# Kernel optimization log

Measured on AMD Instinct MI355X. Metric: run time of the kernel, lower is better.

## Reference

```python
import jax, jax.numpy as jnp
import numpy as np
from jax import lax

WIN = 7            # win_size -> (7,7,7) window in 3d mode
NPIX = WIN ** 3    # 343
K1, K2 = 0.01, 0.03
COV_NORM = NPIX / (NPIX - 1)
DN = ('NCDHW', 'OIDHW', 'NCDHW')


def _box3d(x):
    """Separable uniform (box) mean filter, VALID padding. Same math as
    conv3d with a ones(wt,ws,ws)/NPIX kernel, but O(win) per voxel per axis."""
    kd = jnp.ones((1, 1, WIN, 1, 1), x.dtype)
    kh = jnp.ones((1, 1, 1, WIN, 1), x.dtype)
    kw = jnp.ones((1, 1, 1, 1, WIN), x.dtype)
    x = lax.conv_general_dilated(x, kd, (1, 1, 1), 'VALID', dimension_numbers=DN)
    x = lax.conv_general_dilated(x, kh, (1, 1, 1), 'VALID', dimension_numbers=DN)
    x = lax.conv_general_dilated(x, kw, (1, 1, 1), 'VALID', dimension_numbers=DN)
    return x / NPIX


def setup_inputs() -> dict:
    key = jax.random.key(0)
    k1, k2, k3 = jax.random.split(key, 3)
    shape = (4, 1, 32, 320, 320)  # [B, C=1, T, H, W]
    pred = jax.random.normal(k1, shape, dtype=jnp.float32)
    targ = jax.random.normal(k2, shape, dtype=jnp.float32)
    data_range = jax.random.uniform(k3, (4,), dtype=jnp.float32)
    return {'pred': pred, 'targ': targ, 'data_range': data_range}


def reference(pred, targ, data_range):
    dr = data_range[:, None, None, None, None].astype(pred.dtype)
    C1 = (K1 * dr) ** 2
    C2 = (K2 * dr) ** 2
    ux = _box3d(pred)
    uy = _box3d(targ)
    uxx = _box3d(pred * pred)
    uyy = _box3d(targ * targ)
    uxy = _box3d(pred * targ)
    vx = COV_NORM * (uxx - ux * ux)
    vy = COV_NORM * (uyy - uy * uy)
    vxy = COV_NORM * (uxy - ux * uy)
    A1 = 2 * ux * uy + C1
    A2 = 2 * vxy + C2
    B1 = ux ** 2 + uy ** 2 + C1
    B2 = vx + vy + C2
    S = (A1 * A2) / (B1 * B2)
    return (1 - S).mean()
```

## Files before the change

kernel.cpp:

```cpp
#include <hip/hip_runtime.h>


#define NPIX 343

constexpr int B = 4, T = 32, H = 320, W = 320;
constexpr int TO = T - 6, HO = H - 6, WO = W - 6;
constexpr long long NOUT = (long long)B * TO * HO * WO;

constexpr int TH = 16, TW = 26;
constexpr int IH = 22, IWP = 16;
constexpr int NTH = 20, NTW = 13;
constexpr int NS = 32;

typedef float v2f __attribute__((ext_vector_type(2)));

template<int N>
__device__ __forceinline__ float row_shr(float x) {
    return __int_as_float(__builtin_amdgcn_update_dpp(
        0, __float_as_int(x), 0x110 | N, 0xF, 0xF, true));
}

__global__ __launch_bounds__(256) void ssim3d_fused(
    const float* __restrict__ pred,
    const float* __restrict__ targ,
    const float* __restrict__ drange,
    double* __restrict__ acc)
{
    __shared__ float4 spq[2][IH][IWP];
    __shared__ float wsum[4];

    const int bx = blockIdx.x;
    const int b  = bx / (NTH * NTW);
    int rem      = bx % (NTH * NTW);
    const int h0 = (rem / NTW) * TH;
    const int w0 = (rem % NTW) * TW;

    const int tid = threadIdx.x;
    const int oh  = tid >> 4;
    const int k   = tid & 15;

    const float* pb = pred + (long long)b * T * H * W;
    const float* qb = targ + (long long)b * T * H * W;

    const int r0 = tid >> 4, c0 = tid & 15;
    const int gr0 = min(h0 + r0, H - 1), gc0 = min(w0 + 2 * c0, W - 2);
    const float* g0p = pb + (long long)gr0 * W + gc0;
    const float* g0q = qb + (long long)gr0 * W + gc0;

    const bool act1 = (tid < 96);
    const int r1 = 16 + (tid >> 4), c1 = tid & 15;
    const int gr1 = min(h0 + r1, H - 1), gc1 = min(w0 + 2 * c1, W - 2);
    const float* g1p = pb + (long long)gr1 * W + gc1;
    const float* g1q = qb + (long long)gr1 * W + gc1;

    float2 d0p, d0q, d1p, d1q;
    auto prefetchw = [&](int s) {
        const long long so = (long long)s * H * W;
        d0p = *reinterpret_cast<const float2*>(g0p + so);
        d0q = *reinterpret_cast<const float2*>(g0q + so);
        if (act1) {
            d1p = *reinterpret_cast<const float2*>(g1p + so);
            d1q = *reinterpret_cast<const float2*>(g1q + so);
        }
    };
    auto commitw = [&](int buf) {
        spq[buf][r0][c0] = make_float4(d0p.x, d0p.y, d0q.x, d0q.y);
        if (act1) spq[buf][r1][c1] = make_float4(d1p.x, d1p.y, d1q.x, d1q.y);
    };

    const bool vh = (h0 + oh < HO);
    const bool k3 = (k >= 3);
    const bool vE = k3 && vh && (w0 + 2 * k - 6 < WO);
    const bool vO = k3 && vh && (w0 + 2 * k - 5 < WO);

    const float dr  = drange[b];
    const float C1s = (0.01f * dr) * (0.01f * dr);
    const float C2s = (0.03f * dr) * (0.03f * dr);
    const float inv  = 1.0f / (float)NPIX;
    const float covn = (float)NPIX / (float)(NPIX - 1);
    const v2f invv  = {inv, inv};
    const v2f C1vv  = {C1s, C1s};
    const v2f C2vv  = {C2s, C2s};
    const v2f covnv = {covn, covn};
    const v2f c2cov = {2.f * covn, 2.f * covn};

    v2f rEO[4][7], tEO[4];
#pragma unroll
    for (int f = 0; f < 4; ++f) {
        tEO[f] = (v2f){0.f, 0.f};
#pragma unroll
        for (int j = 0; j < 7; ++j) rEO[f][j] = (v2f){0.f, 0.f};
    }
    float loss = 0.f;

    auto slice = [&](int s, int jj, bool doEmit, bool doCommit, bool doPrefetch) {
        const int bs = s & 1, bn = bs ^ 1;

        if (doCommit)  commitw(bn);
        if (doPrefetch) prefetchw(s + 2);

        v2f c0 = {0.f, 0.f}, c1v = {0.f, 0.f}, c2 = {0.f, 0.f}, c3 = {0.f, 0.f};
#pragma unroll
        for (int dy = 0; dy < 7; ++dy) {
            float4 v = spq[bs][oh + dy][k];
            v2f vp = {v.x, v.y};
            v2f vq = {v.z, v.w};
            c0 += vp;
            c1v += vq;
            c2 = __builtin_elementwise_fma(vp, vp, c2);
            c2 = __builtin_elementwise_fma(vq, vq, c2);
            c3 = __builtin_elementwise_fma(vp, vq, c3);
        }

        __syncthreads();

        v2f sv[4];
        {
            v2f cf[4] = {c0, c1v, c2, c3};
#pragma unroll
            for (int f = 0; f < 4; ++f) {
                float ps = cf[f].x + cf[f].y;
                float t1 = ps + row_shr<1>(ps);
                float s8 = t1 + row_shr<2>(t1);
                float eL = row_shr<3>(cf[f].x);
                sv[f].x = s8 - cf[f].y;
                sv[f].y = s8 - eL;
            }
        }

#pragma unroll
        for (int f = 0; f < 4; ++f) {
            tEO[f] += sv[f] - rEO[f][jj];
            rEO[f][jj] = sv[f];
        }

        if (doEmit) {
            v2f ux  = tEO[0] * invv;
            v2f uy  = tEO[1] * invv;
            v2f u2  = tEO[2] * invv;
            v2f uxy = tEO[3] * invv;
            v2f m   = __builtin_elementwise_fma(-ux, uy, uxy);
            v2f A2  = __builtin_elementwise_fma(c2cov, m, C2vv);
            v2f nb  = __builtin_elementwise_fma(-ux, ux, u2);
            nb      = __builtin_elementwise_fma(-uy, uy, nb);
            v2f B2  = __builtin_elementwise_fma(covnv, nb, C2vv);
            v2f ux2 = ux + ux;
            v2f A1  = __builtin_elementwise_fma(ux2, uy, C1vv);
            v2f B1  = __builtin_elementwise_fma(
                          ux, ux, __builtin_elementwise_fma(uy, uy, C1vv));
            v2f num = A1 * A2;
            v2f den = B1 * B2;
            float sx = __fdividef(num.x, den.x);
            float sy = __fdividef(num.y, den.y);
            if (vE) loss += 1.f - sx;
            if (vO) loss += 1.f - sy;
        }
    };

    prefetchw(0);
    commitw(0);
    prefetchw(1);
    __syncthreads();

#pragma unroll
    for (int jj = 0; jj < 7; ++jj)
        slice(jj, jj, jj == 6, true, true);

    for (int a = 7; a <= 21; a += 7)
#pragma unroll
        for (int jj = 0; jj < 7; ++jj)
            slice(a + jj, jj, true, true, true);

    slice(28, 0, true, true, true);
    slice(29, 1, true, true, true);
    slice(30, 2, true, true, false);
    slice(31, 3, true, false, false);

    for (int off = 32; off > 0; off >>= 1)
        loss += __shfl_down(loss, off, 64);
    const int lane = tid & 63;
    const int wid  = tid >> 6;
    if (lane == 0) wsum[wid] = loss;
    __syncthreads();
    if (tid == 0) {
        float s = wsum[0] + wsum[1] + wsum[2] + wsum[3];
        atomicAdd(acc, (double)s);
    }
}

__global__ void ssim3d_finalize(const double* __restrict__ acc,
                                float* __restrict__ out)
{
    out[0] = (float)(acc[0] / (double)NOUT);
}

extern "C" void kernel_launch(void* const* d_in, const int* in_sizes, int n_in,
                              void* d_out, int out_size, void* d_ws, size_t ws_size,
                              hipStream_t stream)
{
    const float* pred   = (const float*)d_in[0];
    const float* targ   = (const float*)d_in[1];
    const float* drange = (const float*)d_in[2];
    float* out  = (float*)d_out;
    double* acc = (double*)d_ws;

    hipMemsetAsync(acc, 0, sizeof(double), stream);

    const int nblocks = B * NTH * NTW;
    ssim3d_fused<<<nblocks, 256, 0, stream>>>(pred, targ, drange, acc);
    ssim3d_finalize<<<1, 1, 0, stream>>>(acc, out);
}
```

Measured before the change: 72.44 us.

## Use four-slot LDS ring to process two slices per barrier with float4 staging

Grows the shared-memory slice buffer from two slots to four and processes two depth slices per phase, so the kernel needs only half as many block-wide barriers. Global staging switches from float2 loads spread over 256 threads to float4 loads done by 176 threads, which cuts the number of load instructions. In exchange, LDS per block roughly doubles, more loaded data stays live in registers, and the fully unrolled phase loop makes the code larger. Either could lower occupancy.

```diff
diff --git a/kernel.cpp b/kernel.cpp
--- a/kernel.cpp
+++ b/kernel.cpp
@@ -10,7 +10,6 @@
 constexpr int TH = 16, TW = 26;
 constexpr int IH = 22, IWP = 16;
 constexpr int NTH = 20, NTW = 13;
-constexpr int NS = 32;
 
 typedef float v2f __attribute__((ext_vector_type(2)));
 
@@ -26,7 +25,7 @@
     const float* __restrict__ drange,
     double* __restrict__ acc)
 {
-    __shared__ float4 spq[2][IH][IWP];
+    __shared__ float4 spq[4][IH][IWP];
     __shared__ float wsum[4];
 
     const int bx = blockIdx.x;
@@ -42,30 +41,39 @@
     const float* pb = pred + (long long)b * T * H * W;
     const float* qb = targ + (long long)b * T * H * W;
 
-    const int r0 = tid >> 4, c0 = tid & 15;
-    const int gr0 = min(h0 + r0, H - 1), gc0 = min(w0 + 2 * c0, W - 2);
-    const float* g0p = pb + (long long)gr0 * W + gc0;
-    const float* g0q = qb + (long long)gr0 * W + gc0;
-
-    const bool act1 = (tid < 96);
-    const int r1 = 16 + (tid >> 4), c1 = tid & 15;
-    const int gr1 = min(h0 + r1, H - 1), gc1 = min(w0 + 2 * c1, W - 2);
-    const float* g1p = pb + (long long)gr1 * W + gc1;
-    const float* g1q = qb + (long long)gr1 * W + gc1;
-
-    float2 d0p, d0q, d1p, d1q;
-    auto prefetchw = [&](int s) {
-        const long long so = (long long)s * H * W;
-        d0p = *reinterpret_cast<const float2*>(g0p + so);
-        d0q = *reinterpret_cast<const float2*>(g0q + so);
-        if (act1) {
-            d1p = *reinterpret_cast<const float2*>(g1p + so);
-            d1q = *reinterpret_cast<const float2*>(g1q + so);
-        }
-    };
-    auto commitw = [&](int buf) {
-        spq[buf][r0][c0] = make_float4(d0p.x, d0p.y, d0q.x, d0q.y);
-        if (act1) spq[buf][r1][c1] = make_float4(d1p.x, d1p.y, d1q.x, d1q.y);
+    const bool stager = (tid < 176);
+    const int rs = tid >> 3;
+    const int qc = tid & 7;
+    const int grs = min(h0 + rs, H - 1), gcs = min(w0 + 4 * qc, W - 4);
+    const float* gps = pb + (long long)grs * W + gcs;
+    const float* gqs = qb + (long long)grs * W + gcs;
+
+    float4 pA, qA, pB, qB;
+    auto loadA = [&](int s) {
+        if (stager) {
+            const long long so = (long long)s * H * W;
+            pA = *reinterpret_cast<const float4*>(gps + so);
+            qA = *reinterpret_cast<const float4*>(gqs + so);
+        }
+    };
+    auto loadB = [&](int s) {
+        if (stager) {
+            const long long so = (long long)s * H * W;
+            pB = *reinterpret_cast<const float4*>(gps + so);
+            qB = *reinterpret_cast<const float4*>(gqs + so);
+        }
+    };
+    auto commitA = [&](int buf) {
+        if (stager) {
+            spq[buf][rs][2 * qc]     = make_float4(pA.x, pA.y, qA.x, qA.y);
+            spq[buf][rs][2 * qc + 1] = make_float4(pA.z, pA.w, qA.z, qA.w);
+        }
+    };
+    auto commitB = [&](int buf) {
+        if (stager) {
+            spq[buf][rs][2 * qc]     = make_float4(pB.x, pB.y, qB.x, qB.y);
+            spq[buf][rs][2 * qc + 1] = make_float4(pB.z, pB.w, qB.z, qB.w);
+        }
     };
 
     const bool vh = (h0 + oh < HO);
@@ -93,16 +101,11 @@
     }
     float loss = 0.f;
 
-    auto slice = [&](int s, int jj, bool doEmit, bool doCommit, bool doPrefetch) {
-        const int bs = s & 1, bn = bs ^ 1;
-
-        if (doCommit)  commitw(bn);
-        if (doPrefetch) prefetchw(s + 2);
-
+    auto compute = [&](int buf, int jj, bool doEmit) {
         v2f c0 = {0.f, 0.f}, c1v = {0.f, 0.f}, c2 = {0.f, 0.f}, c3 = {0.f, 0.f};
 #pragma unroll
         for (int dy = 0; dy < 7; ++dy) {
-            float4 v = spq[bs][oh + dy][k];
+            float4 v = spq[buf][oh + dy][k];
             v2f vp = {v.x, v.y};
             v2f vq = {v.z, v.w};
             c0 += vp;
@@ -111,8 +114,6 @@
             c2 = __builtin_elementwise_fma(vq, vq, c2);
             c3 = __builtin_elementwise_fma(vp, vq, c3);
         }
-
-        __syncthreads();
 
         v2f sv[4];
         {
@@ -157,24 +158,38 @@
         }
     };
 
-    prefetchw(0);
-    commitw(0);
-    prefetchw(1);
+    auto phase = [&](int p, int jj0, int jj1, bool doEmit,
+                     bool doCommit, bool doPrefetch) {
+        const int s0 = 2 * p;
+        if (doCommit) {
+            commitA((s0 + 2) & 3);
+            commitB((s0 + 3) & 3);
+        }
+        if (doPrefetch) {
+            loadA(s0 + 4);
+            loadB(s0 + 5);
+        }
+        compute(s0 & 3, jj0, doEmit);
+        compute((s0 + 1) & 3, jj1, doEmit);
+        __syncthreads();
+    };
+
+    loadA(0);
+    loadB(1);
+    commitA(0);
+    commitB(1);
+    loadA(2);
+    loadB(3);
     __syncthreads();
 
 #pragma unroll
-    for (int jj = 0; jj < 7; ++jj)
-        slice(jj, jj, jj == 6, true, true);
-
-    for (int a = 7; a <= 21; a += 7)
-#pragma unroll
-        for (int jj = 0; jj < 7; ++jj)
-            slice(a + jj, jj, true, true, true);
-
-    slice(28, 0, true, true, true);
-    slice(29, 1, true, true, true);
-    slice(30, 2, true, true, false);
-    slice(31, 3, true, false, false);
+    for (int p = 0; p < 7; ++p)
+        phase(p, (2 * p) % 7, (2 * p + 1) % 7, p >= 3, true, true);
+#pragma unroll
+    for (int p = 7; p < 14; ++p)
+        phase(p, (2 * p) % 7, (2 * p + 1) % 7, true, true, true);
+    phase(14, 0, 1, true, true, false);
+    phase(15, 2, 3, true, false, false);
 
     for (int off = 32; off > 0; off >>= 1)
         loss += __shfl_down(loss, off, 64);
```

New measurement: 72.72 us. No clear change (+0.4%).

## Give each wavefront a private LDS tile to drop per-slice block barriers

Applied to the files above, without the earlier changes.

The shared-memory tile is split so that each of the four wavefronts stages its own 10-row window: 4 output rows plus a 6-row halo, double-buffered. Each wavefront now reads only data it wrote itself, so the __syncthreads after every depth slice is removed and wavefronts run through the slice loop independently. The price is redundant global loads of halo rows (10 input rows per 4 output rows instead of 22 per 16) and a larger LDS footprint. Correctness relies on in-order LDS access within a single wavefront.

```diff
diff --git a/kernel.cpp b/kernel.cpp
--- a/kernel.cpp
+++ b/kernel.cpp
@@ -8,9 +8,7 @@
 constexpr long long NOUT = (long long)B * TO * HO * WO;
 
 constexpr int TH = 16, TW = 26;
-constexpr int IH = 22, IWP = 16;
 constexpr int NTH = 20, NTW = 13;
-constexpr int NS = 32;
 
 typedef float v2f __attribute__((ext_vector_type(2)));
 
@@ -26,7 +24,7 @@
     const float* __restrict__ drange,
     double* __restrict__ acc)
 {
-    __shared__ float4 spq[2][IH][IWP];
+    __shared__ float4 swv[4][2][10][16];
     __shared__ float wsum[4];
 
     const int bx = blockIdx.x;
@@ -35,40 +33,46 @@
     const int h0 = (rem / NTW) * TH;
     const int w0 = (rem % NTW) * TW;
 
-    const int tid = threadIdx.x;
-    const int oh  = tid >> 4;
-    const int k   = tid & 15;
+    const int tid  = threadIdx.x;
+    const int wv   = tid >> 6;
+    const int lane = tid & 63;
+    const int ohl  = lane >> 4;
+    const int k    = lane & 15;
+    const int h0w  = h0 + 4 * wv;
 
     const float* pb = pred + (long long)b * T * H * W;
     const float* qb = targ + (long long)b * T * H * W;
 
-    const int r0 = tid >> 4, c0 = tid & 15;
-    const int gr0 = min(h0 + r0, H - 1), gc0 = min(w0 + 2 * c0, W - 2);
-    const float* g0p = pb + (long long)gr0 * W + gc0;
-    const float* g0q = qb + (long long)gr0 * W + gc0;
-
-    const bool act1 = (tid < 96);
-    const int r1 = 16 + (tid >> 4), c1 = tid & 15;
-    const int gr1 = min(h0 + r1, H - 1), gc1 = min(w0 + 2 * c1, W - 2);
-    const float* g1p = pb + (long long)gr1 * W + gc1;
-    const float* g1q = qb + (long long)gr1 * W + gc1;
-
-    float2 d0p, d0q, d1p, d1q;
-    auto prefetchw = [&](int s) {
+    const bool has2 = (lane < 32);
+    auto gofs = [&](int i) {
+        int r = min(h0w + (i >> 4), H - 1);
+        int c = min(w0 + 2 * (i & 15), W - 2);
+        return (long long)r * W + c;
+    };
+    const long long ga0 = gofs(lane);
+    const long long ga1 = gofs(lane + 64);
+    const long long ga2 = has2 ? gofs(lane + 128) : 0;
+
+    float2 p0, q0, p1, q1, p2, q2;
+    auto loadw = [&](int s) {
         const long long so = (long long)s * H * W;
-        d0p = *reinterpret_cast<const float2*>(g0p + so);
-        d0q = *reinterpret_cast<const float2*>(g0q + so);
-        if (act1) {
-            d1p = *reinterpret_cast<const float2*>(g1p + so);
-            d1q = *reinterpret_cast<const float2*>(g1q + so);
+        p0 = *reinterpret_cast<const float2*>(pb + so + ga0);
+        q0 = *reinterpret_cast<const float2*>(qb + so + ga0);
+        p1 = *reinterpret_cast<const float2*>(pb + so + ga1);
+        q1 = *reinterpret_cast<const float2*>(qb + so + ga1);
+        if (has2) {
+            p2 = *reinterpret_cast<const float2*>(pb + so + ga2);
+            q2 = *reinterpret_cast<const float2*>(qb + so + ga2);
         }
     };
     auto commitw = [&](int buf) {
-        spq[buf][r0][c0] = make_float4(d0p.x, d0p.y, d0q.x, d0q.y);
-        if (act1) spq[buf][r1][c1] = make_float4(d1p.x, d1p.y, d1q.x, d1q.y);
-    };
-
-    const bool vh = (h0 + oh < HO);
+        swv[wv][buf][ohl][k]     = make_float4(p0.x, p0.y, q0.x, q0.y);
+        swv[wv][buf][4 + ohl][k] = make_float4(p1.x, p1.y, q1.x, q1.y);
+        if (has2)
+            swv[wv][buf][8 + ohl][k] = make_float4(p2.x, p2.y, q2.x, q2.y);
+    };
+
+    const bool vh = (h0w + ohl < HO);
     const bool k3 = (k >= 3);
     const bool vE = k3 && vh && (w0 + 2 * k - 6 < WO);
     const bool vO = k3 && vh && (w0 + 2 * k - 5 < WO);
@@ -94,15 +98,14 @@
     float loss = 0.f;
 
     auto slice = [&](int s, int jj, bool doEmit, bool doCommit, bool doPrefetch) {
-        const int bs = s & 1, bn = bs ^ 1;
-
-        if (doCommit)  commitw(bn);
-        if (doPrefetch) prefetchw(s + 2);
-
+        if (doCommit)  commitw((s + 1) & 1);
+        if (doPrefetch) loadw(s + 2);
+
+        const int bs = s & 1;
         v2f c0 = {0.f, 0.f}, c1v = {0.f, 0.f}, c2 = {0.f, 0.f}, c3 = {0.f, 0.f};
 #pragma unroll
         for (int dy = 0; dy < 7; ++dy) {
-            float4 v = spq[bs][oh + dy][k];
+            float4 v = swv[wv][bs][ohl + dy][k];
             v2f vp = {v.x, v.y};
             v2f vq = {v.z, v.w};
             c0 += vp;
@@ -111,8 +114,6 @@
             c2 = __builtin_elementwise_fma(vq, vq, c2);
             c3 = __builtin_elementwise_fma(vp, vq, c3);
         }
-
-        __syncthreads();
 
         v2f sv[4];
         {
@@ -157,10 +158,9 @@
         }
     };
 
-    prefetchw(0);
+    loadw(0);
     commitw(0);
-    prefetchw(1);
-    __syncthreads();
+    loadw(1);
 
 #pragma unroll
     for (int jj = 0; jj < 7; ++jj)
@@ -178,9 +178,7 @@
 
     for (int off = 32; off > 0; off >>= 1)
         loss += __shfl_down(loss, off, 64);
-    const int lane = tid & 63;
-    const int wid  = tid >> 6;
-    if (lane == 0) wsum[wid] = loss;
+    if (lane == 0) wsum[wv] = loss;
     __syncthreads();
     if (tid == 0) {
         float s = wsum[0] + wsum[1] + wsum[2] + wsum[3];
```

Result: no change. 72.85 us (+0.6%).
